# Kernel tuning notes

Measured on AMD Instinct MI355X. Metric: run time of the kernel, lower is better.

The kernel has to match this reference:

```python
import jax, jax.numpy as jnp
import numpy as np
import math

DIM, H, Q_RANK, KV_RANK = 2048, 16, 768, 512
QK_STATIC, QK_ROT, V_DIM = 128, 64, 128
QK_TOTAL = QK_STATIC + QK_ROT
BS, SEQ = 2, 1024


def rmsnorm(x, scale, eps=1e-6):
    xf = x.astype(jnp.float32)
    return scale * (xf * jax.lax.rsqrt(jnp.mean(xf * xf, axis=-1, keepdims=True) + eps))


def half_rotate(x):
    h = x.shape[-1] // 2
    return jnp.concatenate([-x[..., h:], x[..., :h]], axis=-1)


def rope_tables(seq_len, dim):
    inv_freq = 1.0 / (10000.0 ** (jnp.arange(0, dim, 2, dtype=jnp.float32) / dim))
    freqs = jnp.arange(seq_len, dtype=jnp.float32)[:, None] * inv_freq[None, :]
    cos = jnp.concatenate([jnp.cos(freqs), jnp.cos(freqs)], axis=-1)  # (S, dim)
    sin = jnp.concatenate([jnp.sin(freqs), jnp.sin(freqs)], axis=-1)
    return cos, sin


def setup_inputs() -> dict:
    key = jax.random.key(0)
    ks = jax.random.split(key, 10)
    sc = lambda fan_in: 1.0 / math.sqrt(fan_in)
    x = jax.random.normal(ks[0], (BS, SEQ, DIM), dtype=jnp.float32)
    causal = jnp.where(jnp.tril(jnp.ones((SEQ, SEQ), dtype=bool)), 0.0, -1e9).astype(jnp.float32)
    mask = jnp.broadcast_to(causal[None], (BS, SEQ, SEQ))
    return {
        "x": x,
        "start_pos": 0,
        "mask": mask,
        "q_down_w": jax.random.normal(ks[1], (Q_RANK, DIM)) * sc(DIM),
        "q_down_b": jnp.zeros((Q_RANK,), jnp.float32),
        "q_norm_scale": jnp.ones((Q_RANK,), jnp.float32),
        "q_up_w": jax.random.normal(ks[2], (H * QK_TOTAL, Q_RANK)) * sc(Q_RANK),
        "q_up_b": jnp.zeros((H * QK_TOTAL,), jnp.float32),
        "kv_down_w": jax.random.normal(ks[3], (KV_RANK + QK_ROT, DIM)) * sc(DIM),
        "kv_down_b": jnp.zeros((KV_RANK + QK_ROT,), jnp.float32),
        "kv_norm_scale": jnp.ones((KV_RANK,), jnp.float32),
        "kv_up_w": jax.random.normal(ks[4], (H * (QK_STATIC + V_DIM), KV_RANK)) * sc(KV_RANK),
        "out_w": jax.random.normal(ks[5], (DIM, H * V_DIM)) * sc(H * V_DIM),
        "out_b": jnp.zeros((DIM,), jnp.float32),
    }


def reference(x, start_pos, mask, q_down_w, q_down_b, q_norm_scale, q_up_w, q_up_b,
              kv_down_w, kv_down_b, kv_norm_scale, kv_up_w, out_w, out_b):
    bs, seq_len, _ = x.shape
    # q path: down-proj -> RMSNorm -> up-proj
    q = rmsnorm(x @ q_down_w.T + q_down_b, q_norm_scale)
    q = (q @ q_up_w.T + q_up_b).reshape(bs, seq_len, H, QK_TOTAL)
    q_static, q_rot = q[..., :QK_STATIC], q[..., QK_STATIC:]
    # kv path: shared down-proj producing latent features + rotary key part
    kv = x @ kv_down_w.T + kv_down_b
    kv_feat, k_rot = kv[..., :KV_RANK], kv[..., KV_RANK:]
    # RoPE (original indexes positions 0..seq_len-1)
    cos, sin = rope_tables(seq_len, QK_ROT)
    q_rot = q_rot * cos[None, :, None, :] + half_rotate(q_rot) * sin[None, :, None, :]
    k_rot = k_rot * cos[None, :, :] + half_rotate(k_rot) * sin[None, :, :]  # (b, t, r)
    kv_normed = rmsnorm(kv_feat, kv_norm_scale)  # latent cache contents (b, t, c)
    # matrix absorption: fold kv_up key-weights into q
    w_k_abs = kv_up_w[: H * QK_STATIC, :].reshape(H, QK_STATIC, KV_RANK)
    w_v_abs = kv_up_w[-H * V_DIM :, :].reshape(H, V_DIM, KV_RANK)
    q_static_proj = jnp.einsum('bshd,hdc->bshc', q_static, w_k_abs)
    attn_scores = (jnp.einsum('bshc,btc->bsht', q_static_proj, kv_normed)
                   + jnp.einsum('bshr,btr->bsht', q_rot, k_rot)) / math.sqrt(QK_TOTAL)
    attn_scores = attn_scores + mask[:, :, None, :]
    attn_weights = jax.nn.softmax(attn_scores, axis=-1)
    # attend over latent features, then expand with absorbed value weights
    ctx_c = jnp.einsum('bsht,btc->bshc', attn_weights, kv_normed)
    ctx = jnp.einsum('bshc,hdc->bshd', ctx_c, w_v_abs)
    out = ctx.reshape(bs, seq_len, H * V_DIM) @ out_w.T + out_b
    return out
```

## Files before the change

kernel.cpp:

```cpp
#include <hip/hip_runtime.h>
#include <stdint.h>
#include <stddef.h>


typedef __attribute__((ext_vector_type(8))) short bf16x8;
typedef __attribute__((ext_vector_type(4))) float f32x4;

__device__ inline float b2f(unsigned short v){
    union { unsigned u; float f; } x; x.u = ((unsigned)v) << 16; return x.f;
}
__device__ inline unsigned short f2b(float f){
    union { float f; unsigned u; } x; x.f = f;
    unsigned r = x.u + 0x7fffu + ((x.u >> 16) & 1u);
    return (unsigned short)(r >> 16);
}

__device__ __forceinline__ void gl2lds16(const unsigned short* g, unsigned short* l){
    __builtin_amdgcn_global_load_lds(
        (__attribute__((address_space(1))) void*)const_cast<unsigned short*>(g),
        (__attribute__((address_space(3))) void*)l,
        16, 0, 0);
}

template<typename TC>
__global__ __launch_bounds__(256) void mfma_gemm_bt(
    const unsigned short* __restrict__ A, const unsigned short* __restrict__ B,
    const float* __restrict__ bias, TC* __restrict__ C,
    int M, int N, int K, int lda, int ldb, int ldc,
    int zdiv, long sA_hi, long sA_lo, long sB_hi, long sB_lo, long sC_hi, long sC_lo,
    float alpha, int causal)
{
    int z, bm, bn;
    if (causal & 4){ z = blockIdx.x; bm = blockIdx.y; bn = blockIdx.z; }
    else           { z = blockIdx.z; bm = blockIdx.y; bn = blockIdx.x; }
    int m0, n0;
    if (causal & 1){
        int i = bm;
        int mt = (int)((sqrtf(8.f * i + 1.f) - 1.f) * 0.5f);
        while ((mt + 1) * (mt + 2) / 2 <= i) ++mt;
        while (mt * (mt + 1) / 2 > i) --mt;
        n0 = (i - mt * (mt + 1) / 2) * 128;
        m0 = mt * 128;
    } else { m0 = bm * 128; n0 = bn * 128; }
    if (causal & 2) K = min(K, m0 + 128);

    __shared__ unsigned short As[3][4096];
    __shared__ unsigned short Bs[3][4096];
    const int zh = z / zdiv, zl = z % zdiv;
    A += (size_t)zh * sA_hi + (size_t)zl * sA_lo;
    B += (size_t)zh * sB_hi + (size_t)zl * sB_lo;
    C += (size_t)zh * sC_hi + (size_t)zl * sC_lo;

    const int tid = threadIdx.x, w = tid >> 6, lane = tid & 63;
    const int wm = w >> 1, wn = w & 1;

    const int srow = w * 32 + (lane >> 2);
    const int schunk = ((lane & 3) ^ ((lane >> 3) & 3)) * 8;
    const unsigned short* gA = A + (size_t)(m0 + srow) * lda + schunk;
    const unsigned short* gB = B + (size_t)(n0 + srow) * ldb + schunk;

    const int ktiles = K >> 5;
    auto stage = [&](int buf, int kt){
        const int k0 = kt << 5;
        gl2lds16(gA + k0,            &As[buf][w * 1024]);
        gl2lds16(gA + k0 + 16 * lda, &As[buf][w * 1024 + 512]);
        gl2lds16(gB + k0,            &Bs[buf][w * 1024]);
        gl2lds16(gB + k0 + 16 * ldb, &Bs[buf][w * 1024 + 512]);
    };
    stage(0, 0);
    if (ktiles > 1) stage(1, 1);

    f32x4 acc[4][4] = {};
    const int lm = lane & 15;
    const int kq = (((lane >> 4) ^ (lm >> 1)) & 3) * 8;

    int cur = 0;
    for (int kt = 0; kt < ktiles; ++kt){
        if (kt + 1 < ktiles) __builtin_amdgcn_s_waitcnt(0xF74);
        else                 __builtin_amdgcn_s_waitcnt(0xF70);
        __builtin_amdgcn_s_barrier();
        __asm__ volatile("" ::: "memory");
        if (kt + 2 < ktiles) stage(cur >= 1 ? cur - 1 : 2, kt + 2);
        bf16x8 af[4], bfr[4];
        #pragma unroll
        for (int i = 0; i < 4; ++i)
            af[i] = *(const bf16x8*)&As[cur][(wm * 64 + i * 16 + lm) * 32 + kq];
        #pragma unroll
        for (int j = 0; j < 4; ++j)
            bfr[j] = *(const bf16x8*)&Bs[cur][(wn * 64 + j * 16 + lm) * 32 + kq];
        #pragma unroll
        for (int i = 0; i < 4; ++i)
            #pragma unroll
            for (int j = 0; j < 4; ++j)
                acc[i][j] = __builtin_amdgcn_mfma_f32_16x16x32_bf16(af[i], bfr[j], acc[i][j], 0, 0, 0);
        __asm__ volatile("" ::: "memory");
        cur = (cur == 2) ? 0 : cur + 1;
    }

    #pragma unroll
    for (int i = 0; i < 4; ++i){
        const int m = m0 + wm * 64 + i * 16 + (lane >> 4) * 4;
        #pragma unroll
        for (int j = 0; j < 4; ++j){
            const int n = n0 + wn * 64 + j * 16 + lm;
            if (n < N){
                const float bb = bias ? bias[n] : 0.f;
                #pragma unroll
                for (int r = 0; r < 4; ++r){
                    float v = acc[i][j][r] * alpha + bb;
                    if ((causal & 1) && n > m + r) v = -1e9f;
                    if constexpr (sizeof(TC) == 2)
                        C[(size_t)(m + r) * ldc + n] = (TC)f2b(v);
                    else
                        C[(size_t)(m + r) * ldc + n] = (TC)v;
                }
            }
        }
    }
}

__global__ __launch_bounds__(256) void flash_attn(
    const unsigned short* __restrict__ qu,
    const unsigned short* __restrict__ khcat,
    const unsigned short* __restrict__ vhT,
    unsigned short* __restrict__ ctx)
{
    const int t = blockIdx.x;
    const int k15 = t & 15, kl = k15 & 7;
    int v = (kl & 1) ? (1 + (kl >> 1)) : (8 - (kl >> 1));
    if (k15 & 8) v = 9 - v;
    if (t & 256) v = 9 - v;
    const int o = ((t >> 4) & 15) * 2 + (k15 >> 3) + ((t >> 8) << 5);
    const int mt = 2 * v - 2 + (o & 1);
    const int z  = o >> 1;
    const int b = z >> 4, h = z & 15;
    const int m0 = mt * 64;
    const int nkt = v;

    __shared__ char smem[74240];
    unsigned short (*Qs)[4096] = (unsigned short (*)[4096])smem;
    unsigned short (*Ks)[8192] = (unsigned short (*)[8192])(smem + 24576);
    unsigned short* Ps = (unsigned short*)(smem + 24576);
    float* lrow = (float*)(smem + 73728);

    const unsigned short* kB = khcat + (size_t)z * 196608;
    const unsigned short* vB = vhT + (size_t)z * 131072;

    const int tid = threadIdx.x, w = tid >> 6, lane = tid & 63;
    const int wm = w >> 1, wn = w & 1;
    const int lm = lane & 15, g = lane >> 4;
    const int kq = g * 8;
    const int rs7 = lm & 7;

    if (tid < 128) lrow[tid] = 0.f;

    const int srow8 = lane >> 3;
    const int soff8 = ((lane & 7) ^ (lane >> 3)) * 8;
    const unsigned short* gQ = qu + (size_t)(b * 1024 + m0 + w * 16 + srow8) * 3072
                               + h * 192 + soff8;

    #pragma unroll
    for (int c = 0; c < 3; ++c){
        gl2lds16(gQ + c * 64,            &Qs[c][w * 1024]);
        gl2lds16(gQ + c * 64 + 8 * 3072, &Qs[c][w * 1024 + 512]);
    }

    auto stageK = [&](int buf, int kt, int c){
        const unsigned short* gK = kB + (size_t)(kt * 128 + w * 32 + srow8) * 192
                                   + c * 64 + soff8;
        gl2lds16(gK,            &Ks[buf][w * 2048]);
        gl2lds16(gK + 8 * 192,  &Ks[buf][w * 2048 + 512]);
        gl2lds16(gK + 16 * 192, &Ks[buf][w * 2048 + 1024]);
        gl2lds16(gK + 24 * 192, &Ks[buf][w * 2048 + 1536]);
    };
    stageK(2, 0, 0);

    f32x4 Oacc[2][4] = {};
    const float scl = 0.07216878364870322f;

    for (int kt = 0; kt < nkt; ++kt){
        stageK(0, kt, 1);
        stageK(1, kt, 2);
        __asm__ volatile("" ::: "memory");
        bf16x8 vfr[4][4];
        #pragma unroll
        for (int j = 0; j < 4; ++j)
            #pragma unroll
            for (int kc = 0; kc < 4; ++kc)
                vfr[j][kc] = *(const bf16x8*)(vB + (size_t)(wn * 64 + j * 16 + lm) * 1024
                                              + kt * 128 + kc * 32 + kq);
        __asm__ volatile("" ::: "memory");

        f32x4 S[2][4] = {};
        #pragma unroll
        for (int c = 0; c < 3; ++c){
            if      (c == 0) __builtin_amdgcn_s_waitcnt(0x4F78);
            else if (c == 1) __builtin_amdgcn_s_waitcnt(0x4F74);
            else             __builtin_amdgcn_s_waitcnt(0x4F70);
            __builtin_amdgcn_s_barrier();
            __asm__ volatile("" ::: "memory");
            const int bufc = (c == 0) ? 2 : (c - 1);
            bf16x8 af[2][2], bfr[4][2];
            #pragma unroll
            for (int i = 0; i < 2; ++i)
                #pragma unroll
                for (int kk = 0; kk < 2; ++kk)
                    af[i][kk] = *(const bf16x8*)&Qs[c][(wm * 32 + i * 16 + lm) * 64
                                                       + (((kk * 4 + g) ^ rs7) * 8)];
            #pragma unroll
            for (int j = 0; j < 4; ++j)
                #pragma unroll
                for (int kk = 0; kk < 2; ++kk)
                    bfr[j][kk] = *(const bf16x8*)&Ks[bufc][(wn * 64 + j * 16 + lm) * 64
                                                           + (((kk * 4 + g) ^ rs7) * 8)];
            __builtin_amdgcn_s_setprio(1);
            #pragma unroll
            for (int kk = 0; kk < 2; ++kk)
                #pragma unroll
                for (int i = 0; i < 2; ++i)
                    #pragma unroll
                    for (int j = 0; j < 4; ++j)
                        S[i][j] = __builtin_amdgcn_mfma_f32_16x16x32_bf16(af[i][kk], bfr[j][kk], S[i][j], 0, 0, 0);
            __builtin_amdgcn_s_setprio(0);
            __asm__ volatile("" ::: "memory");
        }
        __builtin_amdgcn_s_waitcnt(0xC07F);
        __builtin_amdgcn_s_barrier();
        __asm__ volatile("" ::: "memory");
        if (kt + 1 < nkt) stageK(2, kt + 1, 0);

        const bool diag = (kt == (mt >> 1));
        #pragma unroll
        for (int i = 0; i < 2; ++i){
            float rs[4] = {0.f, 0.f, 0.f, 0.f};
            #pragma unroll
            for (int j = 0; j < 4; ++j){
                const int nloc = wn * 64 + j * 16 + lm;
                #pragma unroll
                for (int r = 0; r < 4; ++r){
                    const int mloc = wm * 32 + i * 16 + g * 4 + r;
                    float p = __expf(S[i][j][r] * scl);
                    if (diag && (kt * 128 + nloc) > (m0 + mloc)) p = 0.f;
                    rs[r] += p;
                    Ps[mloc * 136 + nloc] = f2b(p);
                }
            }
            #pragma unroll
            for (int r = 0; r < 4; ++r){
                rs[r] += __shfl_xor(rs[r], 1, 64);
                rs[r] += __shfl_xor(rs[r], 2, 64);
                rs[r] += __shfl_xor(rs[r], 4, 64);
                rs[r] += __shfl_xor(rs[r], 8, 64);
            }
            if (lm == 0){
                #pragma unroll
                for (int r = 0; r < 4; ++r)
                    lrow[wn * 64 + wm * 32 + i * 16 + g * 4 + r] += rs[r];
            }
        }
        __asm__ volatile("" ::: "memory");
        __builtin_amdgcn_s_waitcnt(0xC07F);
        __builtin_amdgcn_s_barrier();
        __asm__ volatile("" ::: "memory");

        if (kt + 1 < nkt) __builtin_amdgcn_s_waitcnt(0xF74);
        else              __builtin_amdgcn_s_waitcnt(0xF70);
        #pragma unroll
        for (int kc = 0; kc < 4; ++kc){
            bf16x8 pa[2];
            #pragma unroll
            for (int i = 0; i < 2; ++i)
                pa[i] = *(const bf16x8*)&Ps[(wm * 32 + i * 16 + lm) * 136 + kc * 32 + kq];
            __builtin_amdgcn_s_setprio(1);
            #pragma unroll
            for (int i = 0; i < 2; ++i)
                #pragma unroll
                for (int j = 0; j < 4; ++j)
                    Oacc[i][j] = __builtin_amdgcn_mfma_f32_16x16x32_bf16(pa[i], vfr[j][kc], Oacc[i][j], 0, 0, 0);
            __builtin_amdgcn_s_setprio(0);
        }
        __asm__ volatile("" ::: "memory");
        __builtin_amdgcn_s_waitcnt(0xC07F);
        __builtin_amdgcn_s_barrier();
        __asm__ volatile("" ::: "memory");
    }

    unsigned short* cBase = ctx + ((size_t)(b * 1024 + m0)) * 2048 + h * 128;
    #pragma unroll
    for (int i = 0; i < 2; ++i){
        #pragma unroll
        for (int r = 0; r < 4; ++r){
            const int row = wm * 32 + i * 16 + g * 4 + r;
            const float inv = 1.f / (lrow[row] + lrow[64 + row]);
            #pragma unroll
            for (int j = 0; j < 4; ++j){
                const int col = wn * 64 + j * 16 + lm;
                cBase[(size_t)row * 2048 + col] = f2b(Oacc[i][j][r] * inv);
            }
        }
    }
}

__global__ __launch_bounds__(256) void cast_all(
    const float* __restrict__ s0, unsigned short* __restrict__ d0,
    const float* __restrict__ s1, unsigned short* __restrict__ d1,
    const float* __restrict__ s2, unsigned short* __restrict__ d2,
    const float* __restrict__ s3, unsigned short* __restrict__ d3,
    const float* __restrict__ s4, unsigned short* __restrict__ d4,
    const float* __restrict__ s5, unsigned short* __restrict__ d5)
{
    long i = (long)(blockIdx.x * 256 + threadIdx.x) * 4;
    const float* s; unsigned short* d; long off;
    if      (i <  4194304L){ s = s0; d = d0; off = i; }
    else if (i <  5767168L){ s = s1; d = d1; off = i -  4194304L; }
    else if (i <  8126464L){ s = s2; d = d2; off = i -  5767168L; }
    else if (i <  9306112L){ s = s3; d = d3; off = i -  8126464L; }
    else if (i < 11403264L){ s = s4; d = d4; off = i -  9306112L; }
    else                   { s = s5; d = d5; off = i - 11403264L; }
    float4 v = *(const float4*)(s + off);
    *(ushort4*)(d + off) = make_ushort4(f2b(v.x), f2b(v.y), f2b(v.z), f2b(v.w));
}

__global__ __launch_bounds__(256) void fused_down_post(
    const unsigned short* __restrict__ p,
    const float* __restrict__ q_down_b, const float* __restrict__ kv_down_b,
    const float* __restrict__ q_norm_s, const float* __restrict__ kv_norm_s,
    unsigned short* __restrict__ qn, unsigned short* __restrict__ kcat)
{
    __shared__ float row[1344];
    __shared__ float red[4];
    const int t = blockIdx.x, tid = threadIdx.x;
    const long S = 2752512L;
    const unsigned short* b0 = p + (size_t)t * 1344;
    for (int c = tid; c < 1344; c += 256){
        float v = b2f(b0[c]) + b2f(b0[c + S]) + b2f(b0[c + 2*S]) + b2f(b0[c + 3*S]);
        v += (c < 768) ? q_down_b[c] : kv_down_b[c - 768];
        row[c] = v;
    }
    __syncthreads();
    const int lane = tid & 63, w = tid >> 6;
    float ss = 0.f;
    for (int c = tid; c < 768; c += 256){ float v = row[c]; ss += v * v; }
    #pragma unroll
    for (int o = 32; o > 0; o >>= 1) ss += __shfl_xor(ss, o, 64);
    if (lane == 0) red[w] = ss;
    __syncthreads();
    const float inv1 = rsqrtf((red[0]+red[1]+red[2]+red[3]) / 768.f + 1e-6f);
    __syncthreads();
    ss = 0.f;
    for (int c = tid; c < 512; c += 256){ float v = row[768 + c]; ss += v * v; }
    #pragma unroll
    for (int o = 32; o > 0; o >>= 1) ss += __shfl_xor(ss, o, 64);
    if (lane == 0) red[w] = ss;
    __syncthreads();
    const float inv2 = rsqrtf((red[0]+red[1]+red[2]+red[3]) / 512.f + 1e-6f);
    for (int c = tid; c < 768; c += 256)
        qn[(size_t)t * 768 + c] = f2b(q_norm_s[c] * row[c] * inv1);
    for (int c = tid; c < 512; c += 256)
        kcat[(size_t)t * 576 + c] = f2b(kv_norm_s[c] * row[768 + c] * inv2);
    if (tid < 64){
        const int d = tid, s = t & 1023;
        float x  = row[1280 + d];
        float xp = (d < 32) ? -row[1280 + d + 32] : row[1280 + d - 32];
        float ang = (float)s * powf(10000.f, -(float)(2 * (d & 31)) / 64.f);
        kcat[(size_t)t * 576 + 512 + d] = f2b(x * cosf(ang) + xp * sinf(ang));
    }
}

__global__ __launch_bounds__(256) void reduce_out(
    const unsigned short* __restrict__ p, const float* __restrict__ bias,
    float* __restrict__ out)
{
    const long S = 4194304L;
    long i = (long)(blockIdx.x * 256 + threadIdx.x) * 4;
    ushort4 a = *(const ushort4*)(p + i);
    ushort4 b = *(const ushort4*)(p + i + S);
    float4 bb = *(const float4*)(bias + (i & 2047));
    float4 r = make_float4(b2f(a.x) + b2f(b.x) + bb.x, b2f(a.y) + b2f(b.y) + bb.y,
                           b2f(a.z) + b2f(b.z) + bb.z, b2f(a.w) + b2f(b.w) + bb.w);
    *(float4*)(out + i) = r;
}

__global__ __launch_bounds__(256) void rope_q_krot(
    unsigned short* __restrict__ qu,
    const unsigned short* __restrict__ kcat,
    unsigned short* __restrict__ khcat)
{
    long idx = (long)blockIdx.x * 256 + threadIdx.x;
    if (idx < 1048576L){
        const int d   = idx & 31;
        const int h   = (idx >> 5) & 15;
        const int tok = idx >> 9;
        const int s   = tok & 1023;
        unsigned short* base = qu + (size_t)tok * 3072 + h * 192 + 128;
        float x1 = b2f(base[d]), x2 = b2f(base[d + 32]);
        float ang = (float)s * powf(10000.f, -(float)d / 32.f);
        float c = cosf(ang), sn = sinf(ang);
        base[d]      = f2b(x1 * c - x2 * sn);
        base[d + 32] = f2b(x2 * c + x1 * sn);
    } else {
        idx -= 1048576L;
        const int d   = idx & 63;
        const int h   = (idx >> 6) & 15;
        const int tok = (int)(idx >> 10);
        const int bb  = tok >> 10, s = tok & 1023;
        khcat[((size_t)(bb * 16 + h) * 1024 + s) * 192 + 128 + d] =
            kcat[(size_t)tok * 576 + 512 + d];
    }
}

extern "C" void kernel_launch(void* const* d_in, const int* in_sizes, int n_in,
                              void* d_out, int out_size, void* d_ws, size_t ws_size,
                              hipStream_t stream)
{
    const float* x         = (const float*)d_in[0];
    const float* q_down_w  = (const float*)d_in[3];
    const float* q_down_b  = (const float*)d_in[4];
    const float* q_norm_s  = (const float*)d_in[5];
    const float* q_up_w    = (const float*)d_in[6];
    const float* q_up_b    = (const float*)d_in[7];
    const float* kv_down_w = (const float*)d_in[8];
    const float* kv_down_b = (const float*)d_in[9];
    const float* kv_norm_s = (const float*)d_in[10];
    const float* kv_up_w   = (const float*)d_in[11];
    const float* out_w     = (const float*)d_in[12];
    const float* out_b     = (const float*)d_in[13];
    float* out = (float*)d_out;

    char* ws = (char*)d_ws;
    unsigned short* kvuw  = (unsigned short*)(ws + 0);
    unsigned short* outw  = (unsigned short*)(ws + 4194304);
    unsigned short* kcat  = (unsigned short*)(ws + 12582912);
    unsigned short* vhT   = (unsigned short*)(ws + 14942208);
    unsigned short* khcat = (unsigned short*)(ws + 23330816);
    unsigned short* ctx   = (unsigned short*)(ws + 35913728);
    unsigned short* qu    = (unsigned short*)(ws + 44302336);
    unsigned short* qn    = (unsigned short*)(ws + 56885248);
    unsigned short* p_qkv = (unsigned short*)(ws + 60030976);
    unsigned short* p_out = (unsigned short*)(ws + 60030976);
    unsigned short* xb    = (unsigned short*)(ws + 82051072);
    unsigned short* qkdw  = (unsigned short*)(ws + 90439680);
    unsigned short* quw   = (unsigned short*)(ws + 96206848);

    dim3 blk(256);

    cast_all<<<15232, blk, 0, stream>>>(x, xb, q_down_w, qkdw, q_up_w, quw,
                                        kv_down_w, qkdw + 1572864, kv_up_w, kvuw, out_w, outw);

    mfma_gemm_bt<unsigned short><<<dim3(11, 16, 4), blk, 0, stream>>>(
        xb, qkdw, nullptr, p_qkv, 2048, 1344, 512, 2048, 2048, 1344,
        4, 0L, 512L, 0L, 512L, 0L, 2752512L, 1.0f, 0);
    fused_down_post<<<2048, blk, 0, stream>>>(p_qkv, q_down_b, kv_down_b,
                                              q_norm_s, kv_norm_s, qn, kcat);
    mfma_gemm_bt<unsigned short><<<dim3(24, 16, 1), blk, 0, stream>>>(
        qn, quw, q_up_b, qu, 2048, 3072, 768, 768, 768, 3072,
        1, 0, 0, 0, 0, 0, 0, 1.0f, 0);
    mfma_gemm_bt<unsigned short><<<dim3(32, 1, 8), blk, 0, stream>>>(
        kvuw + 1048576, kcat, nullptr, vhT, 128, 1024, 512, 512, 576, 1024,
        16, 0L, 65536L, 589824L, 0L, 2097152L, 131072L, 1.0f, 4);
    mfma_gemm_bt<unsigned short><<<dim3(32, 8, 1), blk, 0, stream>>>(
        kcat, kvuw, nullptr, khcat, 1024, 128, 512, 576, 512, 192,
        16, 589824L, 0L, 0L, 65536L, 3145728L, 196608L, 1.0f, 4);
    rope_q_krot<<<12288, blk, 0, stream>>>(qu, kcat, khcat);
    flash_attn<<<dim3(512), blk, 0, stream>>>(qu, khcat, vhT, ctx);
    mfma_gemm_bt<unsigned short><<<dim3(16, 16, 2), blk, 0, stream>>>(
        ctx, outw, nullptr, p_out, 2048, 2048, 1024, 2048, 2048, 2048,
        2, 0L, 1024L, 0L, 1024L, 0L, 4194304L, 1.0f, 0);
    reduce_out<<<4096, blk, 0, stream>>>(p_out, out_b, out);
}
```

Baseline: 301.2 us.

## Split long causal query tiles across two blocks with a combine pass

Replaces the old paired scheduling of query tiles with a constant table giving each block a query tile and a KV-tile range. Query tiles 8-15, which have the longest causal KV ranges, are split into two halves that write unnormalized fp32 partial outputs and row sums to a workspace. A new combine_ctx kernel adds the halves and normalizes. The grid grows from 512 to 768 blocks to balance load across CUs, at the cost of extra partial-buffer traffic and one more kernel launch. Because the kernel does not subtract a running max, the two halves can be summed directly without rescaling.

```diff
diff --git a/kernel.cpp b/kernel.cpp
--- a/kernel.cpp
+++ b/kernel.cpp
@@ -119,23 +119,31 @@
     }
 }
 
+__constant__ unsigned short flash_sched[24] = {
+    0x040F, 0x084F, 0x040E, 0x084E, 0x040D, 0x040C, 0x0407, 0x0406,
+    0x074D, 0x074C, 0x030B, 0x063B, 0x030A, 0x063A, 0x0309, 0x0308,
+    0x0305, 0x0304,
+    0x0539, 0x0538, 0x0203, 0x0202,
+    0x0101, 0x0100};
+
 __global__ __launch_bounds__(256) void flash_attn(
     const unsigned short* __restrict__ qu,
     const unsigned short* __restrict__ khcat,
     const unsigned short* __restrict__ vhT,
-    unsigned short* __restrict__ ctx)
+    unsigned short* __restrict__ ctx,
+    float* __restrict__ Opart,
+    float* __restrict__ lpart)
 {
     const int t = blockIdx.x;
-    const int k15 = t & 15, kl = k15 & 7;
-    int v = (kl & 1) ? (1 + (kl >> 1)) : (8 - (kl >> 1));
-    if (k15 & 8) v = 9 - v;
-    if (t & 256) v = 9 - v;
-    const int o = ((t >> 4) & 15) * 2 + (k15 >> 3) + ((t >> 8) << 5);
-    const int mt = 2 * v - 2 + (o & 1);
-    const int z  = o >> 1;
+    const int r8 = t & 7, u = t >> 3;
+    const int s = u >> 2, zg = u & 3;
+    const int z = zg * 8 + r8;
+    const unsigned e = flash_sched[s];
+    const int mt  = e & 15;
+    const int kt0 = (e >> 4) & 15;
+    const int kt1 = (int)(e >> 8);
     const int b = z >> 4, h = z & 15;
     const int m0 = mt * 64;
-    const int nkt = v;
 
     __shared__ char smem[74240];
     unsigned short (*Qs)[4096] = (unsigned short (*)[4096])smem;
@@ -173,12 +181,12 @@
         gl2lds16(gK + 16 * 192, &Ks[buf][w * 2048 + 1024]);
         gl2lds16(gK + 24 * 192, &Ks[buf][w * 2048 + 1536]);
     };
-    stageK(2, 0, 0);
+    stageK(2, kt0, 0);
 
     f32x4 Oacc[2][4] = {};
     const float scl = 0.07216878364870322f;
 
-    for (int kt = 0; kt < nkt; ++kt){
+    for (int kt = kt0; kt < kt1; ++kt){
         stageK(0, kt, 1);
         stageK(1, kt, 2);
         __asm__ volatile("" ::: "memory");
@@ -227,7 +235,7 @@
         __builtin_amdgcn_s_waitcnt(0xC07F);
         __builtin_amdgcn_s_barrier();
         __asm__ volatile("" ::: "memory");
-        if (kt + 1 < nkt) stageK(2, kt + 1, 0);
+        if (kt + 1 < kt1) stageK(2, kt + 1, 0);
 
         const bool diag = (kt == (mt >> 1));
         #pragma unroll
@@ -263,7 +271,7 @@
         __builtin_amdgcn_s_barrier();
         __asm__ volatile("" ::: "memory");
 
-        if (kt + 1 < nkt) __builtin_amdgcn_s_waitcnt(0xF74);
+        if (kt + 1 < kt1) __builtin_amdgcn_s_waitcnt(0xF74);
         else              __builtin_amdgcn_s_waitcnt(0xF70);
         #pragma unroll
         for (int kc = 0; kc < 4; ++kc){
@@ -285,19 +293,70 @@
         __asm__ volatile("" ::: "memory");
     }
 
-    unsigned short* cBase = ctx + ((size_t)(b * 1024 + m0)) * 2048 + h * 128;
+    if (mt < 8){
+        unsigned short* cBase = ctx + ((size_t)(b * 1024 + m0)) * 2048 + h * 128;
+        #pragma unroll
+        for (int i = 0; i < 2; ++i){
+            #pragma unroll
+            for (int r = 0; r < 4; ++r){
+                const int row = wm * 32 + i * 16 + g * 4 + r;
+                const float inv = 1.f / (lrow[row] + lrow[64 + row]);
+                #pragma unroll
+                for (int j = 0; j < 4; ++j){
+                    const int col = wn * 64 + j * 16 + lm;
+                    cBase[(size_t)row * 2048 + col] = f2b(Oacc[i][j][r] * inv);
+                }
+            }
+        }
+    } else {
+        const int p = ((z << 3) + (mt - 8)) * 2 + (kt0 ? 1 : 0);
+        float* Ob = Opart + (size_t)p * 8192;
+        #pragma unroll
+        for (int i = 0; i < 2; ++i){
+            #pragma unroll
+            for (int r = 0; r < 4; ++r){
+                const int row = wm * 32 + i * 16 + g * 4 + r;
+                #pragma unroll
+                for (int j = 0; j < 4; ++j){
+                    const int col = wn * 64 + j * 16 + lm;
+                    Ob[row * 128 + col] = Oacc[i][j][r];
+                }
+            }
+        }
+        if (wn == 0 && lm == 0){
+            #pragma unroll
+            for (int i = 0; i < 2; ++i)
+                #pragma unroll
+                for (int r = 0; r < 4; ++r){
+                    const int row = wm * 32 + i * 16 + g * 4 + r;
+                    lpart[p * 64 + row] = lrow[row] + lrow[64 + row];
+                }
+        }
+    }
+}
+
+__global__ __launch_bounds__(256) void combine_ctx(
+    const float* __restrict__ Opart, const float* __restrict__ lpart,
+    unsigned short* __restrict__ ctx)
+{
+    const int pb = blockIdx.x;
+    const int z = pb >> 3, mt = (pb & 7) + 8;
+    const int b = z >> 4, h = z & 15;
+    const int tid = threadIdx.x;
+    const float* Oa = Opart + (size_t)(2 * pb) * 8192;
+    const float* Ob = Oa + 8192;
+    const float* la = lpart + 2 * pb * 64;
+    unsigned short* cBase = ctx + ((size_t)(b * 1024 + mt * 64)) * 2048 + h * 128;
     #pragma unroll
-    for (int i = 0; i < 2; ++i){
-        #pragma unroll
-        for (int r = 0; r < 4; ++r){
-            const int row = wm * 32 + i * 16 + g * 4 + r;
-            const float inv = 1.f / (lrow[row] + lrow[64 + row]);
-            #pragma unroll
-            for (int j = 0; j < 4; ++j){
-                const int col = wn * 64 + j * 16 + lm;
-                cBase[(size_t)row * 2048 + col] = f2b(Oacc[i][j][r] * inv);
-            }
-        }
+    for (int i = 0; i < 8; ++i){
+        const int idx4 = i * 256 + tid;
+        const int row = idx4 >> 5, c0 = (idx4 & 31) * 4;
+        float4 a  = *(const float4*)(Oa + row * 128 + c0);
+        float4 bv = *(const float4*)(Ob + row * 128 + c0);
+        const float inv = 1.f / (la[row] + la[64 + row]);
+        *(ushort4*)(cBase + (size_t)row * 2048 + c0) = make_ushort4(
+            f2b((a.x + bv.x) * inv), f2b((a.y + bv.y) * inv),
+            f2b((a.z + bv.z) * inv), f2b((a.w + bv.w) * inv));
     }
 }
 
@@ -438,6 +497,8 @@
     unsigned short* qn    = (unsigned short*)(ws + 56885248);
     unsigned short* p_qkv = (unsigned short*)(ws + 60030976);
     unsigned short* p_out = (unsigned short*)(ws + 60030976);
+    float*          Opart = (float*)(ws + 60030976);
+    float*          lpart = (float*)(ws + 76808192);
     unsigned short* xb    = (unsigned short*)(ws + 82051072);
     unsigned short* qkdw  = (unsigned short*)(ws + 90439680);
     unsigned short* quw   = (unsigned short*)(ws + 96206848);
@@ -462,7 +523,8 @@
         kcat, kvuw, nullptr, khcat, 1024, 128, 512, 576, 512, 192,
         16, 589824L, 0L, 0L, 65536L, 3145728L, 196608L, 1.0f, 4);
     rope_q_krot<<<12288, blk, 0, stream>>>(qu, kcat, khcat);
-    flash_attn<<<dim3(512), blk, 0, stream>>>(qu, khcat, vhT, ctx);
+    flash_attn<<<dim3(768), blk, 0, stream>>>(qu, khcat, vhT, ctx, Opart, lpart);
+    combine_ctx<<<dim3(256), blk, 0, stream>>>(Opart, lpart, ctx);
     mfma_gemm_bt<unsigned short><<<dim3(16, 16, 2), blk, 0, stream>>>(
         ctx, outw, nullptr, p_out, 2048, 2048, 1024, 2048, 2048, 2048,
         2, 0L, 1024L, 0L, 1024L, 0L, 4194304L, 1.0f, 0);
```

Measured after the change: 307.8 us. 1.02x slower.

## Merge V/K absorption GEMMs into one launch and drop split-K output reduce

Applied to the files above, without the earlier changes.

Factors the GEMM mainloop into a shared device function and adds a combined kernel that computes the value-transpose and key-absorption products in a single launch, with even and odd blocks picking the task. The output projection now runs as one full-K GEMM that writes fp32 with the bias applied directly. This replaces the two-way split-K with bf16 partials and the separate reduce kernel. It saves two launches and the partial round trip through memory, but the output GEMM now has half as many blocks (256), each with a K loop twice as long.

```diff
diff --git a/kernel.cpp b/kernel.cpp
--- a/kernel.cpp
+++ b/kernel.cpp
@@ -20,6 +20,82 @@
         (__attribute__((address_space(1))) void*)const_cast<unsigned short*>(g),
         (__attribute__((address_space(3))) void*)l,
         16, 0, 0);
+}
+
+template<typename TC>
+static __device__ __forceinline__ void gemm_body(
+    unsigned short (*As)[4096], unsigned short (*Bs)[4096],
+    const unsigned short* A, const unsigned short* B,
+    const float* bias, TC* C,
+    int N, int K, int lda, int ldb, int ldc,
+    int m0, int n0, float alpha, int causal)
+{
+    const int tid = threadIdx.x, w = tid >> 6, lane = tid & 63;
+    const int wm = w >> 1, wn = w & 1;
+
+    const int srow = w * 32 + (lane >> 2);
+    const int schunk = ((lane & 3) ^ ((lane >> 3) & 3)) * 8;
+    const unsigned short* gA = A + (size_t)(m0 + srow) * lda + schunk;
+    const unsigned short* gB = B + (size_t)(n0 + srow) * ldb + schunk;
+
+    const int ktiles = K >> 5;
+    auto stage = [&](int buf, int kt){
+        const int k0 = kt << 5;
+        gl2lds16(gA + k0,            &As[buf][w * 1024]);
+        gl2lds16(gA + k0 + 16 * lda, &As[buf][w * 1024 + 512]);
+        gl2lds16(gB + k0,            &Bs[buf][w * 1024]);
+        gl2lds16(gB + k0 + 16 * ldb, &Bs[buf][w * 1024 + 512]);
+    };
+    stage(0, 0);
+    if (ktiles > 1) stage(1, 1);
+
+    f32x4 acc[4][4] = {};
+    const int lm = lane & 15;
+    const int kq = (((lane >> 4) ^ (lm >> 1)) & 3) * 8;
+
+    int cur = 0;
+    for (int kt = 0; kt < ktiles; ++kt){
+        if (kt + 1 < ktiles) __builtin_amdgcn_s_waitcnt(0xF74);
+        else                 __builtin_amdgcn_s_waitcnt(0xF70);
+        __builtin_amdgcn_s_barrier();
+        __asm__ volatile("" ::: "memory");
+        if (kt + 2 < ktiles) stage(cur >= 1 ? cur - 1 : 2, kt + 2);
+        bf16x8 af[4], bfr[4];
+        #pragma unroll
+        for (int i = 0; i < 4; ++i)
+            af[i] = *(const bf16x8*)&As[cur][(wm * 64 + i * 16 + lm) * 32 + kq];
+        #pragma unroll
+        for (int j = 0; j < 4; ++j)
+            bfr[j] = *(const bf16x8*)&Bs[cur][(wn * 64 + j * 16 + lm) * 32 + kq];
+        #pragma unroll
+        for (int i = 0; i < 4; ++i)
+            #pragma unroll
+            for (int j = 0; j < 4; ++j)
+                acc[i][j] = __builtin_amdgcn_mfma_f32_16x16x32_bf16(af[i], bfr[j], acc[i][j], 0, 0, 0);
+        __asm__ volatile("" ::: "memory");
+        cur = (cur == 2) ? 0 : cur + 1;
+    }
+
+    #pragma unroll
+    for (int i = 0; i < 4; ++i){
+        const int m = m0 + wm * 64 + i * 16 + (lane >> 4) * 4;
+        #pragma unroll
+        for (int j = 0; j < 4; ++j){
+            const int n = n0 + wn * 64 + j * 16 + lm;
+            if (n < N){
+                const float bb = bias ? bias[n] : 0.f;
+                #pragma unroll
+                for (int r = 0; r < 4; ++r){
+                    float v = acc[i][j][r] * alpha + bb;
+                    if ((causal & 1) && n > m + r) v = -1e9f;
+                    if constexpr (sizeof(TC) == 2)
+                        C[(size_t)(m + r) * ldc + n] = (TC)f2b(v);
+                    else
+                        C[(size_t)(m + r) * ldc + n] = (TC)v;
+                }
+            }
+        }
+    }
 }
 
 template<typename TC>
@@ -51,71 +127,31 @@
     B += (size_t)zh * sB_hi + (size_t)zl * sB_lo;
     C += (size_t)zh * sC_hi + (size_t)zl * sC_lo;
 
-    const int tid = threadIdx.x, w = tid >> 6, lane = tid & 63;
-    const int wm = w >> 1, wn = w & 1;
-
-    const int srow = w * 32 + (lane >> 2);
-    const int schunk = ((lane & 3) ^ ((lane >> 3) & 3)) * 8;
-    const unsigned short* gA = A + (size_t)(m0 + srow) * lda + schunk;
-    const unsigned short* gB = B + (size_t)(n0 + srow) * ldb + schunk;
-
-    const int ktiles = K >> 5;
-    auto stage = [&](int buf, int kt){
-        const int k0 = kt << 5;
-        gl2lds16(gA + k0,            &As[buf][w * 1024]);
-        gl2lds16(gA + k0 + 16 * lda, &As[buf][w * 1024 + 512]);
-        gl2lds16(gB + k0,            &Bs[buf][w * 1024]);
-        gl2lds16(gB + k0 + 16 * ldb, &Bs[buf][w * 1024 + 512]);
-    };
-    stage(0, 0);
-    if (ktiles > 1) stage(1, 1);
-
-    f32x4 acc[4][4] = {};
-    const int lm = lane & 15;
-    const int kq = (((lane >> 4) ^ (lm >> 1)) & 3) * 8;
-
-    int cur = 0;
-    for (int kt = 0; kt < ktiles; ++kt){
-        if (kt + 1 < ktiles) __builtin_amdgcn_s_waitcnt(0xF74);
-        else                 __builtin_amdgcn_s_waitcnt(0xF70);
-        __builtin_amdgcn_s_barrier();
-        __asm__ volatile("" ::: "memory");
-        if (kt + 2 < ktiles) stage(cur >= 1 ? cur - 1 : 2, kt + 2);
-        bf16x8 af[4], bfr[4];
-        #pragma unroll
-        for (int i = 0; i < 4; ++i)
-            af[i] = *(const bf16x8*)&As[cur][(wm * 64 + i * 16 + lm) * 32 + kq];
-        #pragma unroll
-        for (int j = 0; j < 4; ++j)
-            bfr[j] = *(const bf16x8*)&Bs[cur][(wn * 64 + j * 16 + lm) * 32 + kq];
-        #pragma unroll
-        for (int i = 0; i < 4; ++i)
-            #pragma unroll
-            for (int j = 0; j < 4; ++j)
-                acc[i][j] = __builtin_amdgcn_mfma_f32_16x16x32_bf16(af[i], bfr[j], acc[i][j], 0, 0, 0);
-        __asm__ volatile("" ::: "memory");
-        cur = (cur == 2) ? 0 : cur + 1;
-    }
-
-    #pragma unroll
-    for (int i = 0; i < 4; ++i){
-        const int m = m0 + wm * 64 + i * 16 + (lane >> 4) * 4;
-        #pragma unroll
-        for (int j = 0; j < 4; ++j){
-            const int n = n0 + wn * 64 + j * 16 + lm;
-            if (n < N){
-                const float bb = bias ? bias[n] : 0.f;
-                #pragma unroll
-                for (int r = 0; r < 4; ++r){
-                    float v = acc[i][j][r] * alpha + bb;
-                    if ((causal & 1) && n > m + r) v = -1e9f;
-                    if constexpr (sizeof(TC) == 2)
-                        C[(size_t)(m + r) * ldc + n] = (TC)f2b(v);
-                    else
-                        C[(size_t)(m + r) * ldc + n] = (TC)v;
-                }
-            }
-        }
+    gemm_body<TC>(As, Bs, A, B, bias, C, N, K, lda, ldb, ldc, m0, n0, alpha, causal);
+}
+
+__global__ __launch_bounds__(256) void mfma_gemm_vk(
+    const unsigned short* __restrict__ kvuw,
+    const unsigned short* __restrict__ kcat,
+    unsigned short* __restrict__ vhT,
+    unsigned short* __restrict__ khcat)
+{
+    __shared__ unsigned short As[3][4096];
+    __shared__ unsigned short Bs[3][4096];
+    const int p = blockIdx.x & 1, z = blockIdx.x >> 1, y = blockIdx.y;
+    const int b = z >> 4, h = z & 15;
+    if (p == 0){
+        const unsigned short* A = kvuw + 1048576 + (size_t)h * 65536;
+        const unsigned short* B = kcat + (size_t)b * 589824;
+        unsigned short* C = vhT + (size_t)b * 2097152 + (size_t)h * 131072;
+        gemm_body<unsigned short>(As, Bs, A, B, nullptr, C,
+                                  1024, 512, 512, 576, 1024, 0, y * 128, 1.0f, 0);
+    } else {
+        const unsigned short* A = kcat + (size_t)b * 589824;
+        const unsigned short* B = kvuw + (size_t)h * 65536;
+        unsigned short* C = khcat + (size_t)b * 3145728 + (size_t)h * 196608;
+        gemm_body<unsigned short>(As, Bs, A, B, nullptr, C,
+                                  128, 512, 576, 512, 192, y * 128, 0, 1.0f, 0);
     }
 }
 
@@ -367,20 +403,6 @@
     }
 }
 
-__global__ __launch_bounds__(256) void reduce_out(
-    const unsigned short* __restrict__ p, const float* __restrict__ bias,
-    float* __restrict__ out)
-{
-    const long S = 4194304L;
-    long i = (long)(blockIdx.x * 256 + threadIdx.x) * 4;
-    ushort4 a = *(const ushort4*)(p + i);
-    ushort4 b = *(const ushort4*)(p + i + S);
-    float4 bb = *(const float4*)(bias + (i & 2047));
-    float4 r = make_float4(b2f(a.x) + b2f(b.x) + bb.x, b2f(a.y) + b2f(b.y) + bb.y,
-                           b2f(a.z) + b2f(b.z) + bb.z, b2f(a.w) + b2f(b.w) + bb.w);
-    *(float4*)(out + i) = r;
-}
-
 __global__ __launch_bounds__(256) void rope_q_krot(
     unsigned short* __restrict__ qu,
     const unsigned short* __restrict__ kcat,
@@ -437,7 +459,6 @@
     unsigned short* qu    = (unsigned short*)(ws + 44302336);
     unsigned short* qn    = (unsigned short*)(ws + 56885248);
     unsigned short* p_qkv = (unsigned short*)(ws + 60030976);
-    unsigned short* p_out = (unsigned short*)(ws + 60030976);
     unsigned short* xb    = (unsigned short*)(ws + 82051072);
     unsigned short* qkdw  = (unsigned short*)(ws + 90439680);
     unsigned short* quw   = (unsigned short*)(ws + 96206848);
@@ -455,16 +476,10 @@
     mfma_gemm_bt<unsigned short><<<dim3(24, 16, 1), blk, 0, stream>>>(
         qn, quw, q_up_b, qu, 2048, 3072, 768, 768, 768, 3072,
         1, 0, 0, 0, 0, 0, 0, 1.0f, 0);
-    mfma_gemm_bt<unsigned short><<<dim3(32, 1, 8), blk, 0, stream>>>(
-        kvuw + 1048576, kcat, nullptr, vhT, 128, 1024, 512, 512, 576, 1024,
-        16, 0L, 65536L, 589824L, 0L, 2097152L, 131072L, 1.0f, 4);
-    mfma_gemm_bt<unsigned short><<<dim3(32, 8, 1), blk, 0, stream>>>(
-        kcat, kvuw, nullptr, khcat, 1024, 128, 512, 576, 512, 192,
-        16, 589824L, 0L, 0L, 65536L, 3145728L, 196608L, 1.0f, 4);
+    mfma_gemm_vk<<<dim3(64, 8, 1), blk, 0, stream>>>(kvuw, kcat, vhT, khcat);
     rope_q_krot<<<12288, blk, 0, stream>>>(qu, kcat, khcat);
     flash_attn<<<dim3(512), blk, 0, stream>>>(qu, khcat, vhT, ctx);
-    mfma_gemm_bt<unsigned short><<<dim3(16, 16, 2), blk, 0, stream>>>(
-        ctx, outw, nullptr, p_out, 2048, 2048, 1024, 2048, 2048, 2048,
-        2, 0L, 1024L, 0L, 1024L, 0L, 4194304L, 1.0f, 0);
-    reduce_out<<<4096, blk, 0, stream>>>(p_out, out_b, out);
-}
+    mfma_gemm_bt<float><<<dim3(16, 16, 1), blk, 0, stream>>>(
+        ctx, outw, out_b, out, 2048, 2048, 2048, 2048, 2048, 2048,
+        1, 0L, 0L, 0L, 0L, 0L, 0L, 1.0f, 0);
+}
```

Result: faster. 293.4 us (-2.6%).
